# Kernel tuning notes

Measured on AMD Instinct MI355X. Metric: run time of the kernel, lower is better.

The kernel has to match this reference:

```python
import jax, jax.numpy as jnp
import numpy as np

EPS = 1e-5
LAMB = 1.0
N_VARS = 40000
N_EDGES = 200000
N_CONF = 100000
FEAT = 128
DOM = 4
T_MAX = 3


def setup_inputs() -> dict:
    key = jax.random.key(0)
    ks = jax.random.split(key, 16)
    # initial node states: torch.rand then row-normalized (F.normalize dim=1)
    s = jax.random.uniform(ks[0], (N_VARS, FEAT), dtype=jnp.float32)
    state0 = s / jnp.maximum(jnp.linalg.norm(s, axis=1, keepdims=True), 1e-12)
    def lin(k, fan_in, shape):
        return jax.random.normal(k, shape, dtype=jnp.float32) / np.sqrt(fan_in)
    inp = {
        'state0': state0,
        'W1': lin(ks[1], 2 * FEAT, (2 * FEAT, FEAT)),
        'b1': jnp.zeros((FEAT,), jnp.float32),
        'W2': lin(ks[2], FEAT, (FEAT, FEAT)),
        'b2': jnp.zeros((FEAT,), jnp.float32),
        'ln_g': jnp.ones((FEAT,), jnp.float32),
        'ln_b': jnp.zeros((FEAT,), jnp.float32),
        'bn_g': jnp.ones((FEAT,), jnp.float32),
        'bn_b': jnp.zeros((FEAT,), jnp.float32),
        'Wd': lin(ks[3], FEAT, (FEAT, DOM)),
        'bd': jnp.zeros((DOM,), jnp.float32),
        # positive relation/confidence matrices so -log(...) is finite
        'relation': jax.random.uniform(ks[4], (DOM, DOM), jnp.float32, 0.1, 1.0),
        'confidence_mat': jax.random.uniform(ks[5], (DOM, DOM), jnp.float32, 0.1, 1.0),
        # positive degrees (divisor)
        'degrees': jax.random.uniform(ks[6], (N_VARS,), jnp.float32, 1.0, 33.0),
        'idx_left': jax.random.randint(ks[7], (N_EDGES,), 0, N_VARS, jnp.int32),
        'idx_right': jax.random.randint(ks[8], (N_EDGES,), 0, N_VARS, jnp.int32),
        'idx_left_pos': jax.random.randint(ks[9], (N_CONF,), 0, N_VARS, jnp.int32),
        'idx_right_pos': jax.random.randint(ks[10], (N_CONF,), 0, N_VARS, jnp.int32),
        'iterations': T_MAX,
    }
    return inp


def reference(state0, W1, b1, W2, b2, ln_g, ln_b, bn_g, bn_b, Wd, bd,
              relation, confidence_mat, degrees,
              idx_left, idx_right, idx_left_pos, idx_right_pos, iterations):
    N, F = state0.shape
    E = idx_left.shape[0]
    degs = degrees[:, None]

    def mlp(x):  # Linear-ReLU-Linear-ReLU-LayerNorm
        h = jax.nn.relu(x @ W1 + b1)
        h = jax.nn.relu(h @ W2 + b2)
        mu = jnp.mean(h, axis=-1, keepdims=True)
        var = jnp.var(h, axis=-1, keepdims=True)  # biased, like torch LayerNorm
        return ln_g * (h - mu) * jax.lax.rsqrt(var + EPS) + ln_b

    state = state0
    logits_list = []
    for _ in range(iterations):
        xl = state[idx_left]          # [E, F] gather
        xr = state[idx_right]
        # mpnn(in_right=xl, in_left=xr): in_lr = cat(xr, xl); in_rl = cat(xl, xr)
        msg = jnp.concatenate([jnp.concatenate([xr, xl], axis=1),
                               jnp.concatenate([xl, xr], axis=1)], axis=0)  # [2E, 2F]
        h = mlp(msg)
        agg = (jnp.zeros((N, F), state.dtype)
               .at[idx_left].add(h[:E])
               .at[idx_right].add(h[E:]))  # scatter-add messages
        rec = agg / degs
        # BatchNorm1d, training mode (batch stats over nodes)
        mu = jnp.mean(rec, axis=0)
        var = jnp.var(rec, axis=0)
        state = bn_g * (rec - mu) * jax.lax.rsqrt(var + EPS) + bn_b
        logits_list.append(state @ Wd + bd)

    phi = jax.nn.softmax(jnp.stack(logits_list, axis=1), axis=2)  # [N, T, D]
    T, D = phi.shape[1], phi.shape[2]
    all_phi = phi.reshape(N, T * D)

    def pair_loss(mat, il, ir, denom):
        pl = all_phi[il].reshape(-1, D)   # [E*T, D]
        pr = all_phi[ir].reshape(-1, D)
        s = jnp.sum((pl @ mat) * pr, axis=1)
        return jnp.sum(-jnp.log(s)) / denom

    n_conflicts = jnp.float32(E)
    n_confidence = jnp.float32(idx_left_pos.shape[0])
    loss = (pair_loss(relation, idx_left, idx_right, n_conflicts)
            + LAMB * pair_loss(confidence_mat, idx_left_pos, idx_right_pos, 10.0 * n_confidence))

    assignment = jnp.argmax(phi, axis=2).astype(jnp.int32)  # [N, T]
    valid = relation[assignment[idx_left], assignment[idx_right]]  # [E, T]
    edge_conflicts = 1.0 - valid
    n_conf = jnp.sum(edge_conflicts[:, -1])
    conflict_ratio = n_conf / n_conflicts
    return (loss, conflict_ratio, phi, edge_conflicts, assignment[:, -1], n_conf)
```

## Files before the change

kernel.cpp:

```cpp
#include <hip/hip_runtime.h>
#include <math.h>

#define N_VARS 40000
#define FEAT 128
#define N_EDGES 200000
#define N_MSG (2*N_EDGES)
#define N_CONFP 100000
#define T_ITERS 3
#define EPSF 1e-5f

#define NB_CONF 782
#define NB_PAIR 1172
#define NB_STAT 157
#define NB_STAT2 625
#define OUT_TOTAL 1120003
#define NCONF_SLOT 1120002

typedef short short8 __attribute__((ext_vector_type(8)));
typedef float floatx4 __attribute__((ext_vector_type(4)));
typedef unsigned short ushort4v __attribute__((ext_vector_type(4)));

__device__ __forceinline__ float scrub0(float x){
  unsigned u = __float_as_uint(x);
  return ((u & 0x7F800000u) == 0x7F800000u) ? 0.f : x;
}
__device__ __forceinline__ unsigned short f2bf_rne(float x){
  unsigned u = __float_as_uint(x);
  u += 0x7FFFu + ((u >> 16) & 1u);
  return (unsigned short)(u >> 16);
}
__device__ __forceinline__ float bf2f(unsigned short h){
  return __uint_as_float(((unsigned)h) << 16);
}
__device__ __forceinline__ unsigned cvtpk(float lo, float hi){
  unsigned r;
  asm("v_cvt_pk_bf16_f32 %0, %1, %2" : "=v"(r) : "v"(lo), "v"(hi));
  return r;
}

__global__ __launch_bounds__(256) void k_zero_int(int* __restrict__ p, int n){
  int i = blockIdx.x*256 + threadIdx.x;
  if (i < n) p[i] = 0;
}

__global__ __launch_bounds__(256) void k_hist(const int* __restrict__ idxL,
    const int* __restrict__ idxR, int* __restrict__ cnt){
  int m = blockIdx.x*256 + threadIdx.x;
  if (m < N_MSG){
    int t = (m < N_EDGES) ? idxL[m] : idxR[m - N_EDGES];
    atomicAdd(&cnt[t], 1);
  }
}
__global__ __launch_bounds__(256) void k_scan1(const int* __restrict__ cnt,
    int* __restrict__ pos, int* __restrict__ blk_tot){
  const int tid = threadIdx.x;
  const int idx = blockIdx.x*256 + tid;
  int v = (idx < N_VARS) ? cnt[idx] : 0;
  __shared__ int sh[256];
  sh[tid] = v;
  __syncthreads();
#pragma unroll
  for (int o = 1; o < 256; o <<= 1){
    int add = (tid >= o) ? sh[tid - o] : 0;
    __syncthreads();
    sh[tid] += add;
    __syncthreads();
  }
  if (idx < N_VARS) pos[idx] = sh[tid] - v;
  if (tid == 255) blk_tot[blockIdx.x] = sh[255];
}
__global__ __launch_bounds__(256) void k_scan2(const int* __restrict__ blk_tot,
    int* __restrict__ blk_off){
  const int tid = threadIdx.x;
  int v = (tid < NB_STAT) ? blk_tot[tid] : 0;
  __shared__ int sh[256];
  sh[tid] = v;
  __syncthreads();
#pragma unroll
  for (int o = 1; o < 256; o <<= 1){
    int add = (tid >= o) ? sh[tid - o] : 0;
    __syncthreads();
    sh[tid] += add;
    __syncthreads();
  }
  if (tid < NB_STAT) blk_off[tid] = sh[tid] - v;
}
__global__ __launch_bounds__(256) void k_scan3(int* __restrict__ pos,
    const int* __restrict__ blk_off){
  const int idx = blockIdx.x*256 + threadIdx.x;
  if (idx < N_VARS) pos[idx] += blk_off[blockIdx.x];
}
__global__ __launch_bounds__(256) void k_fill(const int* __restrict__ idxL,
    const int* __restrict__ idxR, int* __restrict__ pos,
    int* __restrict__ morder, int* __restrict__ nodeof){
  int m = blockIdx.x*256 + threadIdx.x;
  if (m < N_MSG){
    int t = (m < N_EDGES) ? idxL[m] : idxR[m - N_EDGES];
    int slot = atomicAdd(&pos[t], 1);
    morder[slot] = m;
    nodeof[slot] = t;
  }
}

__global__ __launch_bounds__(256) void k_prep2(const float* __restrict__ W2,
                                               const float* __restrict__ W1,
                                               unsigned short* __restrict__ W2pack,
                                               unsigned short* __restrict__ W1pack){
  if (blockIdx.x < 8){
    int gid = blockIdx.x*256 + threadIdx.x;
    int lane = gid & 63;
    int ks = (gid >> 6) & 3;
    int ntg = gid >> 8;
    int kbase = ks*32 + (lane >> 4)*8;
    int n = ntg*16 + (lane & 15);
#pragma unroll
    for (int j = 0; j < 8; ++j)
      W2pack[gid*8 + j] = f2bf_rne(W2[(kbase + j)*FEAT + n]);
  } else {
    int gid = (blockIdx.x - 8)*256 + threadIdx.x;
    int lane = gid & 63;
    int ks = (gid >> 6) & 3;
    int ntg = gid >> 8;
    int kbase = ks*32 + (lane >> 4)*8;
    int n = ntg*16 + (lane & 15);
#pragma unroll
    for (int j = 0; j < 8; ++j){
      int k = kbase + j;
      float v = (n < 128) ? W1[k*FEAT + n] : W1[(128 + k)*FEAT + (n - 128)];
      W1pack[gid*8 + j] = f2bf_rne(v);
    }
  }
}

#define X_STRIDE 136
__global__ __launch_bounds__(256) void k_pq(const float* __restrict__ xf,
                                            const unsigned short* __restrict__ xb,
                                            int src_f32,
                                            const unsigned short* __restrict__ W1pack,
                                            const float* __restrict__ b1v,
                                            unsigned short* __restrict__ PQb,
                                            float* __restrict__ red,
                                            float4* __restrict__ recz){
  __shared__ __align__(16) unsigned short Xbf[32*X_STRIDE];
  const int tid = threadIdx.x;
  const int row0 = blockIdx.x * 32;
  if (blockIdx.x == 0) red[tid] = 0.f;
  {
    const int zid = blockIdx.x*256 + tid;
#pragma unroll
    for (int i = 0; i < 4; ++i)
      recz[zid + i*320000] = make_float4(0.f,0.f,0.f,0.f);
  }
  if (src_f32){
    const int c4 = (tid & 31)*4, g8 = tid >> 5;
#pragma unroll
    for (int r = 0; r < 4; ++r){
      int row = g8*4 + r;
      const float4 v = *(const float4*)&xf[(row0 + row)*FEAT + c4];
      uint2 uu;
      uu.x = cvtpk(v.x, v.y);
      uu.y = cvtpk(v.z, v.w);
      *(uint2*)&Xbf[row*X_STRIDE + c4] = uu;
    }
  } else {
    const int c8 = (tid & 15)*8, g16 = tid >> 4;
#pragma unroll
    for (int r = 0; r < 2; ++r){
      int row = r*16 + g16;
      *(short8*)&Xbf[row*X_STRIDE + c8] = *(const short8*)&xb[(row0 + row)*FEAT + c8];
    }
  }
  __syncthreads();
  const int w = tid >> 6, lane = tid & 63;
  const int quad = lane >> 4, mcol = lane & 15;
  float bi0 = 0.f, bi1 = 0.f, bi2 = 0.f, bi3 = 0.f;
  if (w >= 2){
    int nb = (w - 2)*64 + mcol;
    bi0 = b1v[nb]; bi1 = b1v[nb + 16]; bi2 = b1v[nb + 32]; bi3 = b1v[nb + 48];
  }
#pragma unroll
  for (int mt = 0; mt < 2; ++mt){
    floatx4 a0 = {bi0,bi0,bi0,bi0};
    floatx4 a1 = {bi1,bi1,bi1,bi1};
    floatx4 a2 = {bi2,bi2,bi2,bi2};
    floatx4 a3 = {bi3,bi3,bi3,bi3};
#pragma unroll
    for (int ks = 0; ks < 4; ++ks){
      short8 a = *(const short8*)&Xbf[(mt*16 + mcol)*X_STRIDE + ks*32 + quad*8];
      const unsigned short* bp = W1pack + ((w*16 + ks)*64 + lane)*8;
      short8 b0 = *(const short8*)(bp);
      short8 b1 = *(const short8*)(bp + 2048);
      short8 b2 = *(const short8*)(bp + 4096);
      short8 b3 = *(const short8*)(bp + 6144);
      a0 = __builtin_amdgcn_mfma_f32_16x16x32_bf16(a, b0, a0, 0, 0, 0);
      a1 = __builtin_amdgcn_mfma_f32_16x16x32_bf16(a, b1, a1, 0, 0, 0);
      a2 = __builtin_amdgcn_mfma_f32_16x16x32_bf16(a, b2, a2, 0, 0, 0);
      a3 = __builtin_amdgcn_mfma_f32_16x16x32_bf16(a, b3, a3, 0, 0, 0);
    }
#pragma unroll
    for (int reg = 0; reg < 4; ++reg){
      unsigned u01 = cvtpk(a0[reg], a1[reg]);
      unsigned u23 = cvtpk(a2[reg], a3[reg]);
      size_t base = (size_t)(row0 + mt*16 + quad*4 + reg)*(2*FEAT) + w*64 + mcol;
      PQb[base]      = (unsigned short)u01;
      PQb[base + 16] = (unsigned short)(u01 >> 16);
      PQb[base + 32] = (unsigned short)u23;
      PQb[base + 48] = (unsigned short)(u23 >> 16);
    }
  }
}

#define U_STRIDE 136
#define ZT_STRIDE 68

__global__ __launch_bounds__(256) void k_msgagg(const unsigned short* __restrict__ PQb,
    const unsigned short* __restrict__ W2pack,
    const float* __restrict__ b2v, const float* __restrict__ ln_g, const float* __restrict__ ln_b,
    const int* __restrict__ idxL, const int* __restrict__ idxR,
    const int* __restrict__ morder, const int* __restrict__ nodeof,
    const float* __restrict__ degrees,
    float* __restrict__ rec){
  __shared__ __align__(16) unsigned short Ubf[64*U_STRIDE];
  __shared__ int sTa[64], sTb[64];
  __shared__ float sDinv[64];
  __shared__ int sEdge[2];
  __shared__ unsigned sBrkLo, sBrkHi;
  const int tid = threadIdx.x;
  const int s0 = blockIdx.x * 64;
  if (tid < 64){
    int m = morder[s0 + tid];
    int e = (m < N_EDGES) ? m : (m - N_EDGES);
    int l = idxL[e], r = idxR[e];
    int ta = (m < N_EDGES) ? l : r;
    sTa[tid] = ta;
    sTb[tid] = (m < N_EDGES) ? r : l;
    sDinv[tid] = 1.f / degrees[ta];
  } else if (tid == 64){
    sEdge[0] = (s0 == 0) ? -1 : nodeof[s0 - 1];
  } else if (tid == 65){
    sEdge[1] = (s0 + 64 >= N_MSG) ? -1 : nodeof[s0 + 64];
  }
  __syncthreads();
  if (tid < 64){
    bool d = (tid == 63) ? true : (sTa[tid + 1] != sTa[tid]);
    unsigned long long b = __ballot(d ? 1 : 0);
    if (tid == 0){ sBrkLo = (unsigned)b; sBrkHi = (unsigned)(b >> 32); }
  }
  {
    const int c8 = (tid & 15)*8, g16 = tid >> 4;
    short8 pb[4], qb[4];
#pragma unroll
    for (int r = 0; r < 4; ++r){
      int row = r*16 + g16;
      pb[r] = *(const short8*)&PQb[sTb[row]*(2*FEAT) + c8];
      qb[r] = *(const short8*)&PQb[sTa[row]*(2*FEAT) + FEAT + c8];
    }
#pragma unroll
    for (int r = 0; r < 4; ++r){
      int row = r*16 + g16;
      float f[8];
#pragma unroll
      for (int j = 0; j < 8; ++j)
        f[j] = fmaxf(bf2f((unsigned short)pb[r][j]) + bf2f((unsigned short)qb[r][j]), 0.f);
      uint4 uu;
      uu.x = cvtpk(f[0], f[1]);
      uu.y = cvtpk(f[2], f[3]);
      uu.z = cvtpk(f[4], f[5]);
      uu.w = cvtpk(f[6], f[7]);
      *(uint4*)&Ubf[row*U_STRIDE + c8] = uu;
    }
  }
  __syncthreads();
  const int w = tid >> 6, lane = tid & 63;
  const int quad = lane >> 4, mcol = lane & 15;
  const int rbase = w*16;
  floatx4 acc[8];
#pragma unroll
  for (int nt = 0; nt < 8; ++nt){
    float b = b2v[nt*16 + mcol];
    acc[nt] = (floatx4){b, b, b, b};
  }
#pragma unroll
  for (int ks = 0; ks < 4; ++ks){
    short8 a = *(const short8*)&Ubf[(rbase + mcol)*U_STRIDE + ks*32 + quad*8];
#pragma unroll
    for (int nt = 0; nt < 8; ++nt){
      short8 b = *(const short8*)(W2pack + ((nt*4 + ks)*64 + lane)*8);
      acc[nt] = __builtin_amdgcn_mfma_f32_16x16x32_bf16(a, b, acc[nt], 0, 0, 0);
    }
  }
  float z[8][4];
#pragma unroll
  for (int nt = 0; nt < 8; ++nt){
#pragma unroll
    for (int reg = 0; reg < 4; ++reg) z[nt][reg] = fmaxf(acc[nt][reg], 0.f);
  }
  float ps[4], pq[4];
#pragma unroll
  for (int reg = 0; reg < 4; ++reg){
    ps[reg] = 0.f; pq[reg] = 0.f;
#pragma unroll
    for (int nt = 0; nt < 8; ++nt){
      ps[reg] += z[nt][reg];
      pq[reg] += z[nt][reg]*z[nt][reg];
    }
  }
#pragma unroll
  for (int o = 1; o < 16; o <<= 1){
#pragma unroll
    for (int reg = 0; reg < 4; ++reg){
      ps[reg] += __shfl_xor(ps[reg], o);
      pq[reg] += __shfl_xor(pq[reg], o);
    }
  }
  float lgv[8], lbv[8];
#pragma unroll
  for (int nt = 0; nt < 8; ++nt){
    lgv[nt] = ln_g[nt*16 + mcol];
    lbv[nt] = ln_b[nt*16 + mcol];
  }
  float muv[4], rvv[4];
#pragma unroll
  for (int reg = 0; reg < 4; ++reg){
    float mu = ps[reg] * (1.f/FEAT);
    float var = fmaxf(pq[reg] * (1.f/FEAT) - mu*mu, 0.f);
    muv[reg] = mu;
    rvv[reg] = rsqrtf(var + EPSF);
  }
  unsigned w0p[8], w1p[8];
#pragma unroll
  for (int nt = 0; nt < 8; ++nt){
    float o0 = scrub0(lgv[nt]*(z[nt][0] - muv[0])*rvv[0] + lbv[nt]);
    float o1 = scrub0(lgv[nt]*(z[nt][1] - muv[1])*rvv[1] + lbv[nt]);
    float o2 = scrub0(lgv[nt]*(z[nt][2] - muv[2])*rvv[2] + lbv[nt]);
    float o3 = scrub0(lgv[nt]*(z[nt][3] - muv[3])*rvv[3] + lbv[nt]);
    w0p[nt] = cvtpk(o0, o1);
    w1p[nt] = cvtpk(o2, o3);
  }
  __syncthreads();
#pragma unroll
  for (int nt = 0; nt < 8; ++nt){
    uint2 u; u.x = w0p[nt]; u.y = w1p[nt];
    *(uint2*)&Ubf[(nt*16 + mcol)*ZT_STRIDE + rbase + quad*4] = u;
  }
  __syncthreads();
  {
    const int col = tid & 127, h = tid >> 7;
    const int rbeg = h*32;
    const unsigned bm = __builtin_amdgcn_readfirstlane(h ? sBrkHi : sBrkLo);
    ushort4v rv4[8];
#pragma unroll
    for (int k = 0; k < 8; ++k)
      rv4[k] = *(const ushort4v*)&Ubf[col*ZT_STRIDE + rbeg + k*4];
    float accv = 0.f;
    int cur = sTa[rbeg];
    bool part = (rbeg == 0) ? (sEdge[0] == cur) : (sTa[rbeg-1] == cur);
#pragma unroll
    for (int i = 0; i < 32; ++i){
      accv += bf2f((unsigned short)rv4[i >> 2][i & 3]);
      const bool realbrk = (bm >> i) & 1u;
      if ((i == 31) | realbrk){
        const int r = rbeg + i;
        bool cont = (i == 31) && ((r == 63) ? (sEdge[1] == cur) : !realbrk);
        float v = accv * sDinv[r];
        float* dst = &rec[(size_t)cur*FEAT + col];
        if (part | cont) atomicAdd(dst, v);
        else *dst = v;
        accv = 0.f;
        part = false;
        if (i < 31) cur = sTa[r + 1];
      }
    }
  }
}

__global__ __launch_bounds__(256) void k_edge(const unsigned short* __restrict__ PQb,
    const unsigned short* __restrict__ W2pack,
    const float* __restrict__ b2v, const float* __restrict__ ln_g, const float* __restrict__ ln_b,
    const int* __restrict__ idxL, const int* __restrict__ idxR,
    float* __restrict__ agg){
  __shared__ __align__(16) unsigned short Ubf[32*U_STRIDE];
  __shared__ float sS[64], sQ[64];
  __shared__ int sTa[32], sTb[32];
  const int tid = threadIdx.x;
  const int m0 = blockIdx.x * 32;
  if (tid < 32){
    int m = m0 + tid;
    int e = (m < N_EDGES) ? m : (m - N_EDGES);
    int l = idxL[e], r = idxR[e];
    sTa[tid] = (m < N_EDGES) ? l : r;
    sTb[tid] = (m < N_EDGES) ? r : l;
  }
  __syncthreads();
  {
    const int c8 = (tid & 15)*8, g16 = tid >> 4;
#pragma unroll
    for (int r = 0; r < 2; ++r){
      int row = r*16 + g16;
      short8 pb = *(const short8*)&PQb[sTb[row]*(2*FEAT) + c8];
      short8 qb = *(const short8*)&PQb[sTa[row]*(2*FEAT) + FEAT + c8];
      float f[8];
#pragma unroll
      for (int j = 0; j < 8; ++j)
        f[j] = fmaxf(bf2f((unsigned short)pb[j]) + bf2f((unsigned short)qb[j]), 0.f);
      uint4 uu;
      uu.x = cvtpk(f[0], f[1]);
      uu.y = cvtpk(f[2], f[3]);
      uu.z = cvtpk(f[4], f[5]);
      uu.w = cvtpk(f[6], f[7]);
      *(uint4*)&Ubf[row*U_STRIDE + c8] = uu;
    }
  }
  __syncthreads();
  const int w = tid >> 6, lane = tid & 63;
  const int mt = w & 1, nhalf = w >> 1;
  const int quad = lane >> 4, mcol = lane & 15;
  float bb0 = b2v[nhalf*64 + 0*16 + mcol];
  float bb1 = b2v[nhalf*64 + 1*16 + mcol];
  float bb2 = b2v[nhalf*64 + 2*16 + mcol];
  float bb3 = b2v[nhalf*64 + 3*16 + mcol];
  floatx4 acc0 = {bb0,bb0,bb0,bb0};
  floatx4 acc1 = {bb1,bb1,bb1,bb1};
  floatx4 acc2 = {bb2,bb2,bb2,bb2};
  floatx4 acc3 = {bb3,bb3,bb3,bb3};
#pragma unroll
  for (int ks = 0; ks < 4; ++ks){
    short8 a = *(const short8*)&Ubf[(mt*16 + mcol)*U_STRIDE + ks*32 + quad*8];
    const unsigned short* bp = W2pack + ((nhalf*4*256) + ks*64 + lane)*8;
    short8 bq0 = *(const short8*)(bp);
    short8 bq1 = *(const short8*)(bp + 2048);
    short8 bq2 = *(const short8*)(bp + 4096);
    short8 bq3 = *(const short8*)(bp + 6144);
    acc0 = __builtin_amdgcn_mfma_f32_16x16x32_bf16(a, bq0, acc0, 0, 0, 0);
    acc1 = __builtin_amdgcn_mfma_f32_16x16x32_bf16(a, bq1, acc1, 0, 0, 0);
    acc2 = __builtin_amdgcn_mfma_f32_16x16x32_bf16(a, bq2, acc2, 0, 0, 0);
    acc3 = __builtin_amdgcn_mfma_f32_16x16x32_bf16(a, bq3, acc3, 0, 0, 0);
  }
  float z[4][4];
#pragma unroll
  for (int nt = 0; nt < 4; ++nt){
    floatx4 a4 = (nt == 0) ? acc0 : (nt == 1) ? acc1 : (nt == 2) ? acc2 : acc3;
#pragma unroll
    for (int reg = 0; reg < 4; ++reg) z[nt][reg] = fmaxf(a4[reg], 0.f);
  }
  float ps[4], pq[4];
#pragma unroll
  for (int reg = 0; reg < 4; ++reg){
    ps[reg] = z[0][reg] + z[1][reg] + z[2][reg] + z[3][reg];
    pq[reg] = z[0][reg]*z[0][reg] + z[1][reg]*z[1][reg] + z[2][reg]*z[2][reg] + z[3][reg]*z[3][reg];
  }
#pragma unroll
  for (int o = 1; o < 16; o <<= 1){
#pragma unroll
    for (int reg = 0; reg < 4; ++reg){
      ps[reg] += __shfl_xor(ps[reg], o);
      pq[reg] += __shfl_xor(pq[reg], o);
    }
  }
  if (mcol == 0){
#pragma unroll
    for (int reg = 0; reg < 4; ++reg){
      int row = mt*16 + quad*4 + reg;
      sS[nhalf*32 + row] = ps[reg];
      sQ[nhalf*32 + row] = pq[reg];
    }
  }
  __syncthreads();
  int colv[4]; float lgv[4], lbv[4];
#pragma unroll
  for (int nt = 0; nt < 4; ++nt){
    colv[nt] = nhalf*64 + nt*16 + mcol;
    lgv[nt] = ln_g[colv[nt]];
    lbv[nt] = ln_b[colv[nt]];
  }
#pragma unroll
  for (int reg = 0; reg < 4; ++reg){
    int row = mt*16 + quad*4 + reg;
    float s = sS[row] + sS[32 + row];
    float q = sQ[row] + sQ[32 + row];
    float mu = s * (1.f/FEAT);
    float var = fmaxf(q * (1.f/FEAT) - mu*mu, 0.f);
    float rv = rsqrtf(var + EPSF);
    int a = sTa[row];
#pragma unroll
    for (int nt = 0; nt < 4; ++nt){
      float o = scrub0(lgv[nt]*(z[nt][reg] - mu)*rv + lbv[nt]);
      atomicAdd(&agg[a*FEAT + colv[nt]], o);
    }
  }
}

__global__ __launch_bounds__(256) void k_stats(const float* __restrict__ src,
    const float* __restrict__ degrees, int divide, float* __restrict__ red){
  const int tid = threadIdx.x;
  const int j = tid & 127, half_sel = tid >> 7;
  const int n0 = blockIdx.x * 64;
  float s1 = 0.f, s2 = 0.f;
  for (int i = half_sel; i < 64; i += 2){
    int n = n0 + i;
    float v = src[n*FEAT + j];
    if (divide) v /= degrees[n];
    s1 += v;
    s2 += v*v;
  }
  __shared__ float sh1[256], sh2[256];
  sh1[tid] = s1; sh2[tid] = s2;
  __syncthreads();
  if (half_sel == 0){
    atomicAdd(&red[j],       sh1[tid] + sh1[tid+128]);
    atomicAdd(&red[128 + j], sh2[tid] + sh2[tid+128]);
  }
}

__global__ __launch_bounds__(256) void k_bn(const float* __restrict__ src,
    const float* __restrict__ degrees, int divide, const float* __restrict__ red,
    const float* __restrict__ bn_g, const float* __restrict__ bn_b,
    const float* __restrict__ Wd, const float* __restrict__ bd,
    unsigned short* __restrict__ state_bf, int* __restrict__ asg,
    float* __restrict__ out_phi, float* __restrict__ out_asg, int t){
  const int w = threadIdx.x >> 6, l = threadIdx.x & 63;
  const int n = blockIdx.x*4 + w;
  const float invN = 1.f / (float)N_VARS;
  float mu0 = red[l]*invN,     mu1 = red[l+64]*invN;
  float v0  = fmaxf(red[128+l]*invN    - mu0*mu0, 0.f);
  float v1  = fmaxf(red[128+l+64]*invN - mu1*mu1, 0.f);
  float rv0 = rsqrtf(v0 + EPSF);
  float rv1 = rsqrtf(v1 + EPSF);
  float dinv = divide ? (1.f / degrees[n]) : 1.f;
  float r0 = src[n*FEAT + l]    * dinv;
  float r1 = src[n*FEAT + l+64] * dinv;
  float s0 = scrub0(bn_g[l]   *(r0 - mu0)*rv0 + bn_b[l]);
  float s1 = scrub0(bn_g[l+64]*(r1 - mu1)*rv1 + bn_b[l+64]);
  state_bf[n*FEAT + l]    = f2bf_rne(s0);
  state_bf[n*FEAT + l+64] = f2bf_rne(s1);
  float p[4];
#pragma unroll
  for (int d = 0; d < 4; ++d)
    p[d] = s0*Wd[l*4 + d] + s1*Wd[(l+64)*4 + d];
#pragma unroll
  for (int o = 32; o > 0; o >>= 1){
#pragma unroll
    for (int d = 0; d < 4; ++d) p[d] += __shfl_xor(p[d], o);
  }
  if (l == 0){
    float lg[4];
#pragma unroll
    for (int d = 0; d < 4; ++d) lg[d] = scrub0(p[d] + bd[d]);
    float mx = fmaxf(fmaxf(lg[0],lg[1]), fmaxf(lg[2],lg[3]));
    float ex[4]; float ssum = 0.f;
#pragma unroll
    for (int d = 0; d < 4; ++d){ ex[d] = expf(lg[d] - mx); ssum += ex[d]; }
    float inv = 1.f / ssum;
    int am = 0; float bv = -1.f;
#pragma unroll
    for (int d = 0; d < 4; ++d){
      float pv = scrub0(ex[d]*inv);
      out_phi[n*12 + t*4 + d] = pv;
      if (pv > bv){ bv = pv; am = d; }
    }
    asg[n*3 + t] = am;
    if (t == 2) out_asg[n] = (float)am;
  }
}

__global__ __launch_bounds__(256) void k_lossconf(const float* __restrict__ phi,
    const int* __restrict__ iL, const int* __restrict__ iR,
    const int* __restrict__ iLp, const int* __restrict__ iRp,
    const float* __restrict__ rel, const float* __restrict__ conf,
    const int* __restrict__ asg, float* __restrict__ out_ec,
    float* __restrict__ part_l1, float* __restrict__ part_l2,
    float* __restrict__ part_conf){
  if (blockIdx.x < NB_PAIR){
    const int e = blockIdx.x*256 + threadIdx.x;
    float p1 = 0.f, p2 = 0.f;
    if (e < N_EDGES + N_CONFP){
      const int isrel = (e < N_EDGES);
      const int l = isrel ? iL[e] : iLp[e - N_EDGES];
      const int r = isrel ? iR[e] : iRp[e - N_EDGES];
      const float* M = isrel ? rel : conf;
      const float2* plp = (const float2*)(phi + (size_t)l*12);
      const float2* prp = (const float2*)(phi + (size_t)r*12);
      float L[12], R[12];
#pragma unroll
      for (int k = 0; k < 6; ++k){
        float2 a = plp[k], b = prp[k];
        L[2*k] = a.x; L[2*k+1] = a.y;
        R[2*k] = b.x; R[2*k+1] = b.y;
      }
      float acc = 0.f;
#pragma unroll
      for (int tt = 0; tt < 3; ++tt){
        const float* a = L + tt*4;
        const float* b = R + tt*4;
        float s = 0.f;
#pragma unroll
        for (int j = 0; j < 4; ++j){
          float tj = a[0]*M[0*4+j] + a[1]*M[1*4+j] + a[2]*M[2*4+j] + a[3]*M[3*4+j];
          s += tj*b[j];
        }
        s = scrub0(s); s = fmaxf(s, 1e-35f);
        acc -= __logf(s);
      }
      if (isrel) p1 = acc; else p2 = acc;
    }
    __shared__ float sh1[256], sh2[256];
    sh1[threadIdx.x] = p1; sh2[threadIdx.x] = p2;
    __syncthreads();
    for (int k = 128; k > 0; k >>= 1){
      if (threadIdx.x < k){
        sh1[threadIdx.x] += sh1[threadIdx.x + k];
        sh2[threadIdx.x] += sh2[threadIdx.x + k];
      }
      __syncthreads();
    }
    if (threadIdx.x == 0){
      part_l1[blockIdx.x] = sh1[0];
      part_l2[blockIdx.x] = sh2[0];
    }
  } else {
    const int bid = blockIdx.x - NB_PAIR;
    const int e = bid*256 + threadIdx.x;
    float c2 = 0.f;
    if (e < N_EDGES){
      int l = iL[e], r = iR[e];
#pragma unroll
      for (int tt = 0; tt < 3; ++tt){
        int ai = asg[l*3+tt] & 3, bi = asg[r*3+tt] & 3;
        float c = scrub0(1.f - rel[ai*4 + bi]);
        out_ec[e*3 + tt] = c;
        if (tt == 2) c2 = c;
      }
    }
    __shared__ float sh[256];
    sh[threadIdx.x] = c2;
    __syncthreads();
    for (int k = 128; k > 0; k >>= 1){
      if (threadIdx.x < k) sh[threadIdx.x] += sh[threadIdx.x + k];
      __syncthreads();
    }
    if (threadIdx.x == 0) part_conf[bid] = sh[0];
  }
}

__global__ __launch_bounds__(256) void k_fin(const float* __restrict__ part_conf,
    const float* __restrict__ part_l1, const float* __restrict__ part_l2,
    float* __restrict__ out){
  const int tid = threadIdx.x;
  float a = 0.f, ca = 0.f, b = 0.f, cb = 0.f, c = 0.f;
  for (int i = tid; i < NB_PAIR; i += 256){
    float y = part_l1[i] - ca; float t = a + y; ca = (t - a) - y; a = t;
    float y2 = part_l2[i] - cb; float t2 = b + y2; cb = (t2 - b) - y2; b = t2;
  }
  for (int i = tid; i < NB_CONF; i += 256) c += part_conf[i];
  __shared__ float sh1[256], sh2[256], sh3[256];
  sh1[tid] = a; sh2[tid] = b; sh3[tid] = c;
  __syncthreads();
  for (int k = 128; k > 0; k >>= 1){
    if (tid < k){
      sh1[tid] += sh1[tid + k];
      sh2[tid] += sh2[tid + k];
      sh3[tid] += sh3[tid + k];
    }
    __syncthreads();
  }
  if (tid == 0){
    out[0] = sh1[0]/(float)N_EDGES + sh2[0]/(10.f*(float)N_CONFP);
    float nc = sh3[0];
    out[NCONF_SLOT] = nc;
    out[1] = nc / (float)N_EDGES;
  }
}

extern "C" void kernel_launch(void* const* d_in, const int* in_sizes, int n_in,
                              void* d_out, int out_size, void* d_ws, size_t ws_size,
                              hipStream_t stream){
  const float* state0  = (const float*)d_in[0];
  const float* W1      = (const float*)d_in[1];
  const float* b1v     = (const float*)d_in[2];
  const float* W2      = (const float*)d_in[3];
  const float* b2v     = (const float*)d_in[4];
  const float* ln_g    = (const float*)d_in[5];
  const float* ln_b    = (const float*)d_in[6];
  const float* bn_g    = (const float*)d_in[7];
  const float* bn_b    = (const float*)d_in[8];
  const float* Wd      = (const float*)d_in[9];
  const float* bd      = (const float*)d_in[10];
  const float* rel     = (const float*)d_in[11];
  const float* confm   = (const float*)d_in[12];
  const float* degrees = (const float*)d_in[13];
  const int* idxL = (const int*)d_in[14];
  const int* idxR = (const int*)d_in[15];
  const int* iLp  = (const int*)d_in[16];
  const int* iRp  = (const int*)d_in[17];

  char* ws = (char*)d_ws;
  unsigned short* state_bf = (unsigned short*)(ws);
  unsigned short* PQb  = (unsigned short*)(ws + 10240000);
  float*  recagg    = (float*)(ws + 30720000);
  int*    asg       = (int*)  (ws + 51200000);
  float*  red       = (float*)(ws + 51840768);
  float*  part_l1   = (float*)(ws + 51841792);
  float*  part_l2   = (float*)(ws + 51855860);
  float*  part_conf = (float*)(ws + 51869928);
  unsigned short* W2pack = (unsigned short*)(ws + 51873056);
  unsigned short* W1pack = (unsigned short*)(ws + 51905824);
  int*    pos       = (int*)(ws + 51971360);
  int*    cnt       = (int*)(ws + 52131360);
  int*    morder    = (int*)(ws + 52291360);
  int*    blk_tot   = (int*)(ws + 53891360);
  int*    blk_off   = (int*)(ws + 53892384);
  int*    nodeof    = (int*)(ws + 53893408);
  const int use_csr = (ws_size >= (size_t)55493408) ? 1 : 0;

  float* out     = (float*)d_out;
  float* out_phi = out + 2;
  float* out_ec  = out + 480002;
  float* out_asg = out + 1080002;

  k_prep2<<<24, 256, 0, stream>>>(W2, W1, W2pack, W1pack);

  if (use_csr){
    k_zero_int<<<NB_STAT, 256, 0, stream>>>(cnt, N_VARS);
    k_hist<<<(N_MSG + 255)/256, 256, 0, stream>>>(idxL, idxR, cnt);
    k_scan1<<<NB_STAT, 256, 0, stream>>>(cnt, pos, blk_tot);
    k_scan2<<<1, 256, 0, stream>>>(blk_tot, blk_off);
    k_scan3<<<NB_STAT, 256, 0, stream>>>(pos, blk_off);
    k_fill<<<(N_MSG + 255)/256, 256, 0, stream>>>(idxL, idxR, pos, morder, nodeof);
  }

  for (int t = 0; t < T_ITERS; ++t){
    k_pq<<<N_VARS/32, 256, 0, stream>>>(state0, state_bf, (t == 0) ? 1 : 0, W1pack, b1v,
                                        PQb, red, (float4*)recagg);
    if (use_csr){
      k_msgagg<<<N_MSG/64, 256, 0, stream>>>(PQb, W2pack, b2v, ln_g, ln_b,
                                             idxL, idxR, morder, nodeof, degrees, recagg);
      k_stats<<<NB_STAT2, 256, 0, stream>>>(recagg, degrees, 0, red);
      k_bn<<<N_VARS/4, 256, 0, stream>>>(recagg, degrees, 0, red, bn_g, bn_b, Wd, bd,
                                         state_bf, asg, out_phi, out_asg, t);
    } else {
      k_edge<<<N_MSG/32, 256, 0, stream>>>(PQb, W2pack, b2v, ln_g, ln_b, idxL, idxR, recagg);
      k_stats<<<NB_STAT2, 256, 0, stream>>>(recagg, degrees, 1, red);
      k_bn<<<N_VARS/4, 256, 0, stream>>>(recagg, degrees, 1, red, bn_g, bn_b, Wd, bd,
                                         state_bf, asg, out_phi, out_asg, t);
    }
  }
  k_lossconf<<<NB_PAIR + NB_CONF, 256, 0, stream>>>(out_phi, idxL, idxR, iLp, iRp, rel, confm,
                                                    asg, out_ec, part_l1, part_l2, part_conf);
  k_fin<<<1, 256, 0, stream>>>(part_conf, part_l1, part_l2, out);
}
```

Baseline: 523.4 us.

## Process two 64-message tiles per block with prefetch and packed CSR pairs

The CSR fill now stores a packed (target, other) int2 per slot instead of a message id plus node id. This removes the dependent idxL/idxR gathers in the message-aggregation kernel. Each k_msgagg block now handles 128 messages as two 64-row tiles. The gathers for the second tile are issued before the first tile's MFMA and LayerNorm, so they overlap, and a separate Z buffer in shared memory lets the scatter run alongside the next tile's conversion. The cost is more registers and shared memory per block (launch bounds set to 4), fewer blocks, and a larger workspace for the pairs array.

```diff
diff --git a/kernel.cpp b/kernel.cpp
--- a/kernel.cpp
+++ b/kernel.cpp
@@ -13,6 +13,7 @@
 #define NB_PAIR 1172
 #define NB_STAT 157
 #define NB_STAT2 625
+#define NB_MSGB 3125
 #define OUT_TOTAL 1120003
 #define NCONF_SLOT 1120002
 
@@ -92,13 +93,15 @@
 }
 __global__ __launch_bounds__(256) void k_fill(const int* __restrict__ idxL,
     const int* __restrict__ idxR, int* __restrict__ pos,
-    int* __restrict__ morder, int* __restrict__ nodeof){
+    int2* __restrict__ pairs){
   int m = blockIdx.x*256 + threadIdx.x;
   if (m < N_MSG){
-    int t = (m < N_EDGES) ? idxL[m] : idxR[m - N_EDGES];
+    int e = (m < N_EDGES) ? m : (m - N_EDGES);
+    int l = idxL[e], r = idxR[e];
+    int t = (m < N_EDGES) ? l : r;
+    int o = (m < N_EDGES) ? r : l;
     int slot = atomicAdd(&pos[t], 1);
-    morder[slot] = m;
-    nodeof[slot] = t;
+    pairs[slot] = make_int2(t, o);
   }
 }
 
@@ -213,64 +216,28 @@
 #define U_STRIDE 136
 #define ZT_STRIDE 68
 
-__global__ __launch_bounds__(256) void k_msgagg(const unsigned short* __restrict__ PQb,
-    const unsigned short* __restrict__ W2pack,
-    const float* __restrict__ b2v, const float* __restrict__ ln_g, const float* __restrict__ ln_b,
-    const int* __restrict__ idxL, const int* __restrict__ idxR,
-    const int* __restrict__ morder, const int* __restrict__ nodeof,
-    const float* __restrict__ degrees,
-    float* __restrict__ rec){
-  __shared__ __align__(16) unsigned short Ubf[64*U_STRIDE];
-  __shared__ int sTa[64], sTb[64];
-  __shared__ float sDinv[64];
-  __shared__ int sEdge[2];
-  __shared__ unsigned sBrkLo, sBrkHi;
-  const int tid = threadIdx.x;
-  const int s0 = blockIdx.x * 64;
-  if (tid < 64){
-    int m = morder[s0 + tid];
-    int e = (m < N_EDGES) ? m : (m - N_EDGES);
-    int l = idxL[e], r = idxR[e];
-    int ta = (m < N_EDGES) ? l : r;
-    sTa[tid] = ta;
-    sTb[tid] = (m < N_EDGES) ? r : l;
-    sDinv[tid] = 1.f / degrees[ta];
-  } else if (tid == 64){
-    sEdge[0] = (s0 == 0) ? -1 : nodeof[s0 - 1];
-  } else if (tid == 65){
-    sEdge[1] = (s0 + 64 >= N_MSG) ? -1 : nodeof[s0 + 64];
-  }
-  __syncthreads();
-  if (tid < 64){
-    bool d = (tid == 63) ? true : (sTa[tid + 1] != sTa[tid]);
-    unsigned long long b = __ballot(d ? 1 : 0);
-    if (tid == 0){ sBrkLo = (unsigned)b; sBrkHi = (unsigned)(b >> 32); }
-  }
-  {
-    const int c8 = (tid & 15)*8, g16 = tid >> 4;
-    short8 pb[4], qb[4];
-#pragma unroll
-    for (int r = 0; r < 4; ++r){
-      int row = r*16 + g16;
-      pb[r] = *(const short8*)&PQb[sTb[row]*(2*FEAT) + c8];
-      qb[r] = *(const short8*)&PQb[sTa[row]*(2*FEAT) + FEAT + c8];
-    }
-#pragma unroll
-    for (int r = 0; r < 4; ++r){
-      int row = r*16 + g16;
-      float f[8];
-#pragma unroll
-      for (int j = 0; j < 8; ++j)
-        f[j] = fmaxf(bf2f((unsigned short)pb[r][j]) + bf2f((unsigned short)qb[r][j]), 0.f);
-      uint4 uu;
-      uu.x = cvtpk(f[0], f[1]);
-      uu.y = cvtpk(f[2], f[3]);
-      uu.z = cvtpk(f[4], f[5]);
-      uu.w = cvtpk(f[6], f[7]);
-      *(uint4*)&Ubf[row*U_STRIDE + c8] = uu;
-    }
-  }
-  __syncthreads();
+__device__ __forceinline__ void conv_store_U(const short8* pb, const short8* qb,
+                                             unsigned short* Ubf, int c8, int g16){
+#pragma unroll
+  for (int r = 0; r < 4; ++r){
+    int row = r*16 + g16;
+    float f[8];
+#pragma unroll
+    for (int j = 0; j < 8; ++j)
+      f[j] = fmaxf(bf2f((unsigned short)pb[r][j]) + bf2f((unsigned short)qb[r][j]), 0.f);
+    uint4 uu;
+    uu.x = cvtpk(f[0], f[1]);
+    uu.y = cvtpk(f[2], f[3]);
+    uu.z = cvtpk(f[4], f[5]);
+    uu.w = cvtpk(f[6], f[7]);
+    *(uint4*)&Ubf[row*U_STRIDE + c8] = uu;
+  }
+}
+
+__device__ __forceinline__ void mfma_ln_zt(const unsigned short* Ubf,
+    unsigned short* Zbf, const unsigned short* __restrict__ W2pack,
+    const float* __restrict__ b2v, const float* __restrict__ ln_g,
+    const float* __restrict__ ln_b, int tid){
   const int w = tid >> 6, lane = tid & 63;
   const int quad = lane >> 4, mcol = lane & 15;
   const int rbase = w*16;
@@ -312,12 +279,6 @@
       ps[reg] += __shfl_xor(ps[reg], o);
       pq[reg] += __shfl_xor(pq[reg], o);
     }
-  }
-  float lgv[8], lbv[8];
-#pragma unroll
-  for (int nt = 0; nt < 8; ++nt){
-    lgv[nt] = ln_g[nt*16 + mcol];
-    lbv[nt] = ln_b[nt*16 + mcol];
   }
   float muv[4], rvv[4];
 #pragma unroll
@@ -327,51 +288,107 @@
     muv[reg] = mu;
     rvv[reg] = rsqrtf(var + EPSF);
   }
-  unsigned w0p[8], w1p[8];
 #pragma unroll
   for (int nt = 0; nt < 8; ++nt){
-    float o0 = scrub0(lgv[nt]*(z[nt][0] - muv[0])*rvv[0] + lbv[nt]);
-    float o1 = scrub0(lgv[nt]*(z[nt][1] - muv[1])*rvv[1] + lbv[nt]);
-    float o2 = scrub0(lgv[nt]*(z[nt][2] - muv[2])*rvv[2] + lbv[nt]);
-    float o3 = scrub0(lgv[nt]*(z[nt][3] - muv[3])*rvv[3] + lbv[nt]);
-    w0p[nt] = cvtpk(o0, o1);
-    w1p[nt] = cvtpk(o2, o3);
-  }
-  __syncthreads();
-#pragma unroll
-  for (int nt = 0; nt < 8; ++nt){
-    uint2 u; u.x = w0p[nt]; u.y = w1p[nt];
-    *(uint2*)&Ubf[(nt*16 + mcol)*ZT_STRIDE + rbase + quad*4] = u;
-  }
-  __syncthreads();
-  {
-    const int col = tid & 127, h = tid >> 7;
-    const int rbeg = h*32;
-    const unsigned bm = __builtin_amdgcn_readfirstlane(h ? sBrkHi : sBrkLo);
-    ushort4v rv4[8];
-#pragma unroll
-    for (int k = 0; k < 8; ++k)
-      rv4[k] = *(const ushort4v*)&Ubf[col*ZT_STRIDE + rbeg + k*4];
-    float accv = 0.f;
-    int cur = sTa[rbeg];
-    bool part = (rbeg == 0) ? (sEdge[0] == cur) : (sTa[rbeg-1] == cur);
-#pragma unroll
-    for (int i = 0; i < 32; ++i){
-      accv += bf2f((unsigned short)rv4[i >> 2][i & 3]);
-      const bool realbrk = (bm >> i) & 1u;
-      if ((i == 31) | realbrk){
-        const int r = rbeg + i;
-        bool cont = (i == 31) && ((r == 63) ? (sEdge[1] == cur) : !realbrk);
-        float v = accv * sDinv[r];
-        float* dst = &rec[(size_t)cur*FEAT + col];
-        if (part | cont) atomicAdd(dst, v);
-        else *dst = v;
-        accv = 0.f;
-        part = false;
-        if (i < 31) cur = sTa[r + 1];
-      }
-    }
-  }
+    float lg = ln_g[nt*16 + mcol];
+    float lb = ln_b[nt*16 + mcol];
+    float o0 = scrub0(lg*(z[nt][0] - muv[0])*rvv[0] + lb);
+    float o1 = scrub0(lg*(z[nt][1] - muv[1])*rvv[1] + lb);
+    float o2 = scrub0(lg*(z[nt][2] - muv[2])*rvv[2] + lb);
+    float o3 = scrub0(lg*(z[nt][3] - muv[3])*rvv[3] + lb);
+    uint2 u; u.x = cvtpk(o0, o1); u.y = cvtpk(o2, o3);
+    *(uint2*)&Zbf[(nt*16 + mcol)*ZT_STRIDE + rbase + quad*4] = u;
+  }
+}
+
+__device__ __forceinline__ void phaseC(const unsigned short* Zbf,
+    const int* sTa_t, const float* sDinv_t, const unsigned* brk2,
+    int eprev, int enext, float* __restrict__ rec, int tid){
+  const int col = tid & 127, h = tid >> 7;
+  const int rbeg = h*32;
+  const unsigned bm = __builtin_amdgcn_readfirstlane(brk2[h]);
+  ushort4v rv4[8];
+#pragma unroll
+  for (int k = 0; k < 8; ++k)
+    rv4[k] = *(const ushort4v*)&Zbf[col*ZT_STRIDE + rbeg + k*4];
+  float accv = 0.f;
+  int cur = sTa_t[rbeg];
+  bool part = (rbeg == 0) ? (eprev == cur) : (sTa_t[rbeg-1] == cur);
+#pragma unroll
+  for (int i = 0; i < 32; ++i){
+    accv += bf2f((unsigned short)rv4[i >> 2][i & 3]);
+    const bool realbrk = (bm >> i) & 1u;
+    if ((i == 31) | realbrk){
+      const int r = rbeg + i;
+      bool cont = (i == 31) && ((r == 63) ? (enext == cur) : !realbrk);
+      float v = accv * sDinv_t[r];
+      float* dst = &rec[(size_t)cur*FEAT + col];
+      if (part | cont) atomicAdd(dst, v);
+      else *dst = v;
+      accv = 0.f;
+      part = false;
+      if (i < 31) cur = sTa_t[r + 1];
+    }
+  }
+}
+
+__global__ __launch_bounds__(256, 4) void k_msgagg(const unsigned short* __restrict__ PQb,
+    const unsigned short* __restrict__ W2pack,
+    const float* __restrict__ b2v, const float* __restrict__ ln_g, const float* __restrict__ ln_b,
+    const int2* __restrict__ pairs, const float* __restrict__ degrees,
+    float* __restrict__ rec){
+  __shared__ __align__(16) unsigned short Ubf[64*U_STRIDE];
+  __shared__ __align__(16) unsigned short Zbf[128*ZT_STRIDE];
+  __shared__ int sTa[2][64];
+  __shared__ float sDinv[2][64];
+  __shared__ int sE[2][2];
+  __shared__ unsigned sBrk[2][2];
+  const int tid = threadIdx.x;
+  const int s0 = blockIdx.x * 128;
+  const int c8 = (tid & 15)*8, g16 = tid >> 4;
+  int2 prA[4], prB[4];
+#pragma unroll
+  for (int r = 0; r < 4; ++r){
+    prA[r] = pairs[s0 + r*16 + g16];
+    prB[r] = pairs[s0 + 64 + r*16 + g16];
+  }
+  short8 pbA[4], qbA[4];
+#pragma unroll
+  for (int r = 0; r < 4; ++r){
+    pbA[r] = *(const short8*)&PQb[(size_t)prA[r].y*(2*FEAT) + c8];
+    qbA[r] = *(const short8*)&PQb[(size_t)prA[r].x*(2*FEAT) + FEAT + c8];
+  }
+  const int w = tid >> 6, lane = tid & 63;
+  if (w == 1 || w == 2){
+    const int tl = w - 1;
+    int ta = pairs[s0 + tl*64 + lane].x;
+    sTa[tl][lane] = ta;
+    sDinv[tl][lane] = 1.f / degrees[ta];
+    int tn = __shfl_down(ta, 1);
+    bool d = (lane == 63) ? true : (tn != ta);
+    unsigned long long b = __ballot(d);
+    if (lane == 0){ sBrk[tl][0] = (unsigned)b; sBrk[tl][1] = (unsigned)(b >> 32); }
+  } else if (w == 3 && lane < 4){
+    int tl = lane >> 1, sd = lane & 1;
+    int idx = s0 + tl*64 + (sd ? 64 : -1);
+    sE[tl][sd] = (idx < 0 || idx >= N_MSG) ? -1 : pairs[idx].x;
+  }
+  conv_store_U(pbA, qbA, Ubf, c8, g16);
+  short8 pbB[4], qbB[4];
+#pragma unroll
+  for (int r = 0; r < 4; ++r){
+    pbB[r] = *(const short8*)&PQb[(size_t)prB[r].y*(2*FEAT) + c8];
+    qbB[r] = *(const short8*)&PQb[(size_t)prB[r].x*(2*FEAT) + FEAT + c8];
+  }
+  __syncthreads();
+  mfma_ln_zt(Ubf, Zbf, W2pack, b2v, ln_g, ln_b, tid);
+  __syncthreads();
+  phaseC(Zbf, sTa[0], sDinv[0], sBrk[0], sE[0][0], sE[0][1], rec, tid);
+  conv_store_U(pbB, qbB, Ubf, c8, g16);
+  __syncthreads();
+  mfma_ln_zt(Ubf, Zbf, W2pack, b2v, ln_g, ln_b, tid);
+  __syncthreads();
+  phaseC(Zbf, sTa[1], sDinv[1], sBrk[1], sE[1][0], sE[1][1], rec, tid);
 }
 
 __global__ __launch_bounds__(256) void k_edge(const unsigned short* __restrict__ PQb,
@@ -706,10 +723,9 @@
   unsigned short* W1pack = (unsigned short*)(ws + 51905824);
   int*    pos       = (int*)(ws + 51971360);
   int*    cnt       = (int*)(ws + 52131360);
-  int*    morder    = (int*)(ws + 52291360);
-  int*    blk_tot   = (int*)(ws + 53891360);
-  int*    blk_off   = (int*)(ws + 53892384);
-  int*    nodeof    = (int*)(ws + 53893408);
+  int2*   pairs     = (int2*)(ws + 52291360);
+  int*    blk_tot   = (int*)(ws + 55491360);
+  int*    blk_off   = (int*)(ws + 55492384);
   const int use_csr = (ws_size >= (size_t)55493408) ? 1 : 0;
 
   float* out     = (float*)d_out;
@@ -725,15 +741,15 @@
     k_scan1<<<NB_STAT, 256, 0, stream>>>(cnt, pos, blk_tot);
     k_scan2<<<1, 256, 0, stream>>>(blk_tot, blk_off);
     k_scan3<<<NB_STAT, 256, 0, stream>>>(pos, blk_off);
-    k_fill<<<(N_MSG + 255)/256, 256, 0, stream>>>(idxL, idxR, pos, morder, nodeof);
+    k_fill<<<(N_MSG + 255)/256, 256, 0, stream>>>(idxL, idxR, pos, pairs);
   }
 
   for (int t = 0; t < T_ITERS; ++t){
     k_pq<<<N_VARS/32, 256, 0, stream>>>(state0, state_bf, (t == 0) ? 1 : 0, W1pack, b1v,
                                         PQb, red, (float4*)recagg);
     if (use_csr){
-      k_msgagg<<<N_MSG/64, 256, 0, stream>>>(PQb, W2pack, b2v, ln_g, ln_b,
-                                             idxL, idxR, morder, nodeof, degrees, recagg);
+      k_msgagg<<<NB_MSGB, 256, 0, stream>>>(PQb, W2pack, b2v, ln_g, ln_b,
+                                            pairs, degrees, recagg);
       k_stats<<<NB_STAT2, 256, 0, stream>>>(recagg, degrees, 0, red);
       k_bn<<<N_VARS/4, 256, 0, stream>>>(recagg, degrees, 0, red, bn_g, bn_b, Wd, bd,
                                          state_bf, asg, out_phi, out_asg, t);
```

Measured after the change: 552.3 us. 5.5% more time.

## Zero only boundary aggregation rows and stage PQ output through LDS

Applied to the files above, without the earlier changes.

Stops zeroing the full 20 MB aggregation buffer on every iteration. A new pass lists nodes with zero degree or whose message segment spans a 64-message block boundary, and k_pq zeroes only those rows. This relies on k_msgagg writing every other row directly rather than accumulating into it. k_pq also stages its bf16 output tile in shared memory so global stores become coalesced 16-byte writes instead of scattered 2-byte stores. This adds a boundary-detection kernel and extra syncs, and the boundary list is capped at a fixed size.

```diff
diff --git a/kernel.cpp b/kernel.cpp
--- a/kernel.cpp
+++ b/kernel.cpp
@@ -13,6 +13,8 @@
 #define NB_PAIR 1172
 #define NB_STAT 157
 #define NB_STAT2 625
+#define NB_MSG64 6250
+#define BND_MAX 16384
 #define OUT_TOTAL 1120003
 #define NCONF_SLOT 1120002
 
@@ -41,6 +43,9 @@
 __global__ __launch_bounds__(256) void k_zero_int(int* __restrict__ p, int n){
   int i = blockIdx.x*256 + threadIdx.x;
   if (i < n) p[i] = 0;
+}
+__global__ __launch_bounds__(256) void k_zero_agg(float4* __restrict__ p){
+  p[blockIdx.x*256 + threadIdx.x] = make_float4(0.f,0.f,0.f,0.f);
 }
 
 __global__ __launch_bounds__(256) void k_hist(const int* __restrict__ idxL,
@@ -70,8 +75,9 @@
   if (tid == 255) blk_tot[blockIdx.x] = sh[255];
 }
 __global__ __launch_bounds__(256) void k_scan2(const int* __restrict__ blk_tot,
-    int* __restrict__ blk_off){
+    int* __restrict__ blk_off, int* __restrict__ bnd_cnt){
   const int tid = threadIdx.x;
+  if (tid == 0) *bnd_cnt = 0;
   int v = (tid < NB_STAT) ? blk_tot[tid] : 0;
   __shared__ int sh[256];
   sh[tid] = v;
@@ -99,6 +105,24 @@
     int slot = atomicAdd(&pos[t], 1);
     morder[slot] = m;
     nodeof[slot] = t;
+  }
+}
+__global__ __launch_bounds__(256) void k_bfind(const int* __restrict__ nodeof,
+    const int* __restrict__ cnt, int* __restrict__ list, int* __restrict__ lcnt){
+  int i = blockIdx.x*256 + threadIdx.x;
+  if (i < N_VARS && cnt[i] == 0){
+    int p = atomicAdd(lcnt, 1);
+    if (p < BND_MAX) list[p] = i;
+  }
+  if (i < NB_MSG64){
+    if (nodeof[i*64 + 31] == nodeof[i*64 + 32]){
+      int p = atomicAdd(lcnt, 1);
+      if (p < BND_MAX) list[p] = nodeof[i*64 + 32];
+    }
+    if (i > 0 && nodeof[i*64 - 1] == nodeof[i*64]){
+      int p = atomicAdd(lcnt, 1);
+      if (p < BND_MAX) list[p] = nodeof[i*64];
+    }
   }
 }
 
@@ -133,6 +157,7 @@
 }
 
 #define X_STRIDE 136
+#define PQ_OSTRIDE 264
 __global__ __launch_bounds__(256) void k_pq(const float* __restrict__ xf,
                                             const unsigned short* __restrict__ xb,
                                             int src_f32,
@@ -140,16 +165,21 @@
                                             const float* __restrict__ b1v,
                                             unsigned short* __restrict__ PQb,
                                             float* __restrict__ red,
-                                            float4* __restrict__ recz){
-  __shared__ __align__(16) unsigned short Xbf[32*X_STRIDE];
+                                            float* __restrict__ rec,
+                                            const int* __restrict__ bnd_list,
+                                            const int* __restrict__ bnd_cnt,
+                                            int zero_list){
+  __shared__ __align__(16) unsigned short S[32*PQ_OSTRIDE];
   const int tid = threadIdx.x;
   const int row0 = blockIdx.x * 32;
   if (blockIdx.x == 0) red[tid] = 0.f;
-  {
-    const int zid = blockIdx.x*256 + tid;
-#pragma unroll
-    for (int i = 0; i < 4; ++i)
-      recz[zid + i*320000] = make_float4(0.f,0.f,0.f,0.f);
+  if (zero_list){
+    const int g = blockIdx.x*256 + tid;
+    const int bc = min(*bnd_cnt, BND_MAX);
+    for (int ri = g >> 5; ri < bc; ri += 10000){
+      int n = bnd_list[ri];
+      ((float4*)(rec + (size_t)n*FEAT))[g & 31] = make_float4(0.f,0.f,0.f,0.f);
+    }
   }
   if (src_f32){
     const int c4 = (tid & 31)*4, g8 = tid >> 5;
@@ -160,14 +190,14 @@
       uint2 uu;
       uu.x = cvtpk(v.x, v.y);
       uu.y = cvtpk(v.z, v.w);
-      *(uint2*)&Xbf[row*X_STRIDE + c4] = uu;
+      *(uint2*)&S[row*X_STRIDE + c4] = uu;
     }
   } else {
     const int c8 = (tid & 15)*8, g16 = tid >> 4;
 #pragma unroll
     for (int r = 0; r < 2; ++r){
       int row = r*16 + g16;
-      *(short8*)&Xbf[row*X_STRIDE + c8] = *(const short8*)&xb[(row0 + row)*FEAT + c8];
+      *(short8*)&S[row*X_STRIDE + c8] = *(const short8*)&xb[(row0 + row)*FEAT + c8];
     }
   }
   __syncthreads();
@@ -178,6 +208,7 @@
     int nb = (w - 2)*64 + mcol;
     bi0 = b1v[nb]; bi1 = b1v[nb + 16]; bi2 = b1v[nb + 32]; bi3 = b1v[nb + 48];
   }
+  floatx4 A[2][4];
 #pragma unroll
   for (int mt = 0; mt < 2; ++mt){
     floatx4 a0 = {bi0,bi0,bi0,bi0};
@@ -186,7 +217,7 @@
     floatx4 a3 = {bi3,bi3,bi3,bi3};
 #pragma unroll
     for (int ks = 0; ks < 4; ++ks){
-      short8 a = *(const short8*)&Xbf[(mt*16 + mcol)*X_STRIDE + ks*32 + quad*8];
+      short8 a = *(const short8*)&S[(mt*16 + mcol)*X_STRIDE + ks*32 + quad*8];
       const unsigned short* bp = W1pack + ((w*16 + ks)*64 + lane)*8;
       short8 b0 = *(const short8*)(bp);
       short8 b1 = *(const short8*)(bp + 2048);
@@ -197,16 +228,30 @@
       a2 = __builtin_amdgcn_mfma_f32_16x16x32_bf16(a, b2, a2, 0, 0, 0);
       a3 = __builtin_amdgcn_mfma_f32_16x16x32_bf16(a, b3, a3, 0, 0, 0);
     }
+    A[mt][0] = a0; A[mt][1] = a1; A[mt][2] = a2; A[mt][3] = a3;
+  }
+  __syncthreads();
+#pragma unroll
+  for (int mt = 0; mt < 2; ++mt){
 #pragma unroll
     for (int reg = 0; reg < 4; ++reg){
-      unsigned u01 = cvtpk(a0[reg], a1[reg]);
-      unsigned u23 = cvtpk(a2[reg], a3[reg]);
-      size_t base = (size_t)(row0 + mt*16 + quad*4 + reg)*(2*FEAT) + w*64 + mcol;
-      PQb[base]      = (unsigned short)u01;
-      PQb[base + 16] = (unsigned short)(u01 >> 16);
-      PQb[base + 32] = (unsigned short)u23;
-      PQb[base + 48] = (unsigned short)(u23 >> 16);
-    }
+      unsigned u01 = cvtpk(A[mt][0][reg], A[mt][1][reg]);
+      unsigned u23 = cvtpk(A[mt][2][reg], A[mt][3][reg]);
+      int row = mt*16 + quad*4 + reg;
+      int cb = w*64 + mcol;
+      S[row*PQ_OSTRIDE + cb]      = (unsigned short)u01;
+      S[row*PQ_OSTRIDE + cb + 16] = (unsigned short)(u01 >> 16);
+      S[row*PQ_OSTRIDE + cb + 32] = (unsigned short)u23;
+      S[row*PQ_OSTRIDE + cb + 48] = (unsigned short)(u23 >> 16);
+    }
+  }
+  __syncthreads();
+  {
+    const int orow = tid >> 3, ocg = (tid & 7)*32;
+    const size_t gbase = (size_t)(row0 + orow)*(2*FEAT) + ocg;
+#pragma unroll
+    for (int j = 0; j < 4; ++j)
+      *(short8*)&PQb[gbase + j*8] = *(const short8*)&S[orow*PQ_OSTRIDE + ocg + j*8];
   }
 }
 
@@ -710,7 +755,9 @@
   int*    blk_tot   = (int*)(ws + 53891360);
   int*    blk_off   = (int*)(ws + 53892384);
   int*    nodeof    = (int*)(ws + 53893408);
-  const int use_csr = (ws_size >= (size_t)55493408) ? 1 : 0;
+  int*    bnd_list  = (int*)(ws + 55493408);
+  int*    bnd_cnt   = (int*)(ws + 55558944);
+  const int use_csr = (ws_size >= (size_t)55558948) ? 1 : 0;
 
   float* out     = (float*)d_out;
   float* out_phi = out + 2;
@@ -723,21 +770,23 @@
     k_zero_int<<<NB_STAT, 256, 0, stream>>>(cnt, N_VARS);
     k_hist<<<(N_MSG + 255)/256, 256, 0, stream>>>(idxL, idxR, cnt);
     k_scan1<<<NB_STAT, 256, 0, stream>>>(cnt, pos, blk_tot);
-    k_scan2<<<1, 256, 0, stream>>>(blk_tot, blk_off);
+    k_scan2<<<1, 256, 0, stream>>>(blk_tot, blk_off, bnd_cnt);
     k_scan3<<<NB_STAT, 256, 0, stream>>>(pos, blk_off);
     k_fill<<<(N_MSG + 255)/256, 256, 0, stream>>>(idxL, idxR, pos, morder, nodeof);
+    k_bfind<<<NB_STAT, 256, 0, stream>>>(nodeof, cnt, bnd_list, bnd_cnt);
   }
 
   for (int t = 0; t < T_ITERS; ++t){
     k_pq<<<N_VARS/32, 256, 0, stream>>>(state0, state_bf, (t == 0) ? 1 : 0, W1pack, b1v,
-                                        PQb, red, (float4*)recagg);
+                                        PQb, red, recagg, bnd_list, bnd_cnt, use_csr);
     if (use_csr){
-      k_msgagg<<<N_MSG/64, 256, 0, stream>>>(PQb, W2pack, b2v, ln_g, ln_b,
+      k_msgagg<<<NB_MSG64, 256, 0, stream>>>(PQb, W2pack, b2v, ln_g, ln_b,
                                              idxL, idxR, morder, nodeof, degrees, recagg);
       k_stats<<<NB_STAT2, 256, 0, stream>>>(recagg, degrees, 0, red);
       k_bn<<<N_VARS/4, 256, 0, stream>>>(recagg, degrees, 0, red, bn_g, bn_b, Wd, bd,
                                          state_bf, asg, out_phi, out_asg, t);
     } else {
+      k_zero_agg<<<5000, 256, 0, stream>>>((float4*)recagg);
       k_edge<<<N_MSG/32, 256, 0, stream>>>(PQb, W2pack, b2v, ln_g, ln_b, idxL, idxR, recagg);
       k_stats<<<NB_STAT2, 256, 0, stream>>>(recagg, degrees, 1, red);
       k_bn<<<N_VARS/4, 256, 0, stream>>>(recagg, degrees, 1, red, bn_g, bn_b, Wd, bd,
```

New measurement: 524.2 us. About the same (+0.1%).
